# Kernel tuning notes

Measured on AMD Instinct MI355X. Metric: run time of the kernel, lower is better.

Reference implementation:

```python
import jax, jax.numpy as jnp
import numpy as np

TEMPERATURE = 0.5

def setup_inputs() -> dict:
    key = jax.random.key(0)
    k1, k2 = jax.random.split(key)
    N, D = 4096, 128
    emb_i = jax.random.normal(k1, (N, D), dtype=jnp.float32)
    emb_j = jax.random.normal(k2, (N, D), dtype=jnp.float32)
    return {"emb_i": emb_i, "emb_j": emb_j}

def reference(emb_i, emb_j):
    # L2-normalize each embedding (F.normalize, dim=1)
    z_i = emb_i / jnp.linalg.norm(emb_i, axis=1, keepdims=True)
    z_j = emb_j / jnp.linalg.norm(emb_j, axis=1, keepdims=True)
    N = z_j.shape[0]
    reps = jnp.concatenate([z_i, z_j], axis=0)  # [2N, D], unit rows
    # cosine similarity of unit vectors == dot product
    logits = jnp.einsum('id,jd->ij', reps, reps) / TEMPERATURE  # [2N, 2N]
    # denominator excludes only k == i (self), positive pair included
    diag_mask = jnp.eye(2 * N, dtype=bool)
    masked = jnp.where(diag_mask, -jnp.inf, logits)
    lse = jax.nn.logsumexp(masked, axis=1)  # [2N]
    # positive index: i <-> i+N
    pos_idx = jnp.concatenate([jnp.arange(N) + N, jnp.arange(N)])
    pos_logits = jnp.take_along_axis(logits, pos_idx[:, None], axis=1)[:, 0]
    # loss = mean over all 2N anchors of -(log numerator - log denominator)
    loss = jnp.mean(lse - pos_logits)
    return loss
```

## Files before the change

### kernel.cpp

```cpp
#include <hip/hip_runtime.h>
#include <hip/hip_bf16.h>

#define NROW 4096
#define D 128
#define TOT 8192
#define PRESCALE 1.69864407f

typedef __attribute__((ext_vector_type(8))) short bf16x8;
typedef __attribute__((ext_vector_type(4))) float f32x4;

__device__ __forceinline__ float fast_exp2(float x) {
#if __has_builtin(__builtin_amdgcn_exp2f)
  return __builtin_amdgcn_exp2f(x);
#else
  return exp2f(x);
#endif
}
__device__ __forceinline__ float fast_log2(float x) {
#if __has_builtin(__builtin_amdgcn_logf)
  return __builtin_amdgcn_logf(x);
#else
  return log2f(x);
#endif
}

__device__ __forceinline__ unsigned short f2bf(float x) {
  unsigned u = __float_as_uint(x);
  unsigned r = (u + 0x7fffu + ((u >> 16) & 1u)) >> 16;
  return (unsigned short)r;
}

__global__ __launch_bounds__(256) void k_norm(
    const float* __restrict__ ei, const float* __restrict__ ej,
    unsigned short* __restrict__ Zp, float* __restrict__ pos) {
  int wid = threadIdx.x >> 6;
  int lane = threadIdx.x & 63;
  int r = blockIdx.x * 4 + wid;
  const float2 xi = *(const float2*)(ei + (size_t)r * D + lane * 2);
  const float2 xj = *(const float2*)(ej + (size_t)r * D + lane * 2);
  float si = xi.x * xi.x + xi.y * xi.y;
  float sj = xj.x * xj.x + xj.y * xj.y;
  float dd = xi.x * xj.x + xi.y * xj.y;
#pragma unroll
  for (int m = 32; m >= 1; m >>= 1) {
    si += __shfl_xor(si, m, 64);
    sj += __shfl_xor(sj, m, 64);
    dd += __shfl_xor(dd, m, 64);
  }
  float ri = rsqrtf(si); ri = ri * (1.5f - 0.5f * si * ri * ri);
  float rj = rsqrtf(sj); rj = rj * (1.5f - 0.5f * sj * rj * rj);
  unsigned short a0 = f2bf(xi.x * ri * PRESCALE);
  unsigned short a1 = f2bf(xi.y * ri * PRESCALE);
  unsigned short b0 = f2bf(xj.x * rj * PRESCALE);
  unsigned short b1 = f2bf(xj.y * rj * PRESCALE);
  unsigned wa = (unsigned)a0 | ((unsigned)a1 << 16);
  unsigned wb = (unsigned)b0 | ((unsigned)b1 << 16);
  ((unsigned*)(Zp + (size_t)r * D))[lane] = wa;
  ((unsigned*)(Zp + (size_t)(r + NROW) * D))[lane] = wb;
  if (lane == 0) pos[r] = 2.0f * dd * ri * rj;
}

#define RG 32
#define CS 32
#define CPB (TOT / CS)
__global__ __launch_bounds__(256) void k_gemm(
    const unsigned short* __restrict__ Zp, float* __restrict__ rowsum) {
  int wid = threadIdx.x >> 6;
  int lane = threadIdx.x & 63;
  int lo = lane & 15, hi = lane >> 4;
  int rb = blockIdx.x & (RG - 1);
  int cs = blockIdx.x >> 5;
  int rowbase = rb * 256 + wid * 64;

  bf16x8 af[4][4];
#pragma unroll
  for (int g = 0; g < 4; ++g) {
    const unsigned short* za = Zp + (size_t)(rowbase + g * 16 + lo) * D + hi * 8;
#pragma unroll
    for (int kk = 0; kk < 4; ++kk)
      af[g][kk] = *(const bf16x8*)(za + kk * 32);
  }

  float sums[4][4];
#pragma unroll
  for (int g = 0; g < 4; ++g)
#pragma unroll
    for (int r = 0; r < 4; ++r) sums[g][r] = 0.0f;

  bool blkdiag = (cs == rb);
#pragma unroll 4
  for (int t = 0; t < CPB / 16; ++t) {
    int colbase = cs * CPB + t * 16;
    const unsigned short* zb = Zp + (size_t)(colbase + lo) * D + hi * 8;
    bf16x8 bf[4];
#pragma unroll
    for (int kk = 0; kk < 4; ++kk)
      bf[kk] = *(const bf16x8*)(zb + kk * 32);
    int gd = t - wid * 4;
#pragma unroll
    for (int g = 0; g < 4; ++g) {
      f32x4 acc = {0.0f, 0.0f, 0.0f, 0.0f};
#pragma unroll
      for (int kk = 0; kk < 4; ++kk)
        acc = __builtin_amdgcn_mfma_f32_16x16x32_bf16(af[g][kk], bf[kk], acc, 0, 0, 0);
      if (blkdiag && g == gd) {
#pragma unroll
        for (int r = 0; r < 4; ++r) {
          float e = (lo == hi * 4 + r) ? 0.0f : fast_exp2(acc[r]);
          sums[g][r] += e;
        }
      } else {
#pragma unroll
        for (int r = 0; r < 4; ++r) sums[g][r] += fast_exp2(acc[r]);
      }
    }
  }

#pragma unroll
  for (int g = 0; g < 4; ++g)
#pragma unroll
    for (int r = 0; r < 4; ++r) {
      float v = sums[g][r];
      v += __shfl_xor(v, 1, 64);
      v += __shfl_xor(v, 2, 64);
      v += __shfl_xor(v, 4, 64);
      v += __shfl_xor(v, 8, 64);
      if (lo == 0) atomicAdd(&rowsum[rowbase + g * 16 + hi * 4 + r], v);
    }
}

__global__ __launch_bounds__(256) void k_final(
    const float* __restrict__ rowsum, const float* __restrict__ pos,
    float* __restrict__ out) {
  int idx = blockIdx.x * 256 + (int)threadIdx.x;
  float lse = fast_log2(rowsum[idx]) * 0.69314718055994531f;
  float c = lse * (1.0f / (float)TOT);
  if (idx < NROW) c -= pos[idx] * (1.0f / (float)NROW);
#pragma unroll
  for (int m = 32; m >= 1; m >>= 1) c += __shfl_xor(c, m, 64);
  __shared__ float ws[4];
  int wid = threadIdx.x >> 6, lane = threadIdx.x & 63;
  if (lane == 0) ws[wid] = c;
  __syncthreads();
  if (threadIdx.x == 0) atomicAdd(out, ws[0] + ws[1] + ws[2] + ws[3]);
}

extern "C" void kernel_launch(void* const* d_in, const int* in_sizes, int n_in,
                              void* d_out, int out_size, void* d_ws, size_t ws_size,
                              hipStream_t stream) {
  const float* ei = (const float*)d_in[0];
  const float* ej = (const float*)d_in[1];
  float* out = (float*)d_out;
  float* rowsum = (float*)d_ws;
  float* pos = (float*)((char*)d_ws + TOT * 4);
  unsigned short* Zp =
      (unsigned short*)((char*)d_ws + TOT * 4 + NROW * 4);

  hipMemsetAsync(out, 0, sizeof(float), stream);
  hipMemsetAsync(rowsum, 0, TOT * sizeof(float), stream);
  k_norm<<<NROW / 4, 256, 0, stream>>>(ei, ej, Zp, pos);
  k_gemm<<<RG * CS, 256, 0, stream>>>(Zp, rowsum);
  k_final<<<TOT / 256, 256, 0, stream>>>(rowsum, pos, out);
}
```

Before: 108.0 us.

## Stage column tiles via async LDS loads, fuse finalize, drop memsets

```diff
diff --git a/kernel.cpp b/kernel.cpp
--- a/kernel.cpp
+++ b/kernel.cpp
@@ -5,6 +5,9 @@
 #define D 128
 #define TOT 8192
 #define PRESCALE 1.69864407f
+#define GRID_G 1024
+#define CPB 256
+#define NT 16
 
 typedef __attribute__((ext_vector_type(8))) short bf16x8;
 typedef __attribute__((ext_vector_type(4))) float f32x4;
@@ -30,9 +33,20 @@
   return (unsigned short)r;
 }
 
+__device__ __forceinline__ void gload16(const void* g, void* l) {
+  __builtin_amdgcn_global_load_lds(
+      (const __attribute__((address_space(1))) unsigned int*)g,
+      (__attribute__((address_space(3))) unsigned int*)l, 16, 0, 0);
+}
+
 __global__ __launch_bounds__(256) void k_norm(
     const float* __restrict__ ei, const float* __restrict__ ej,
-    unsigned short* __restrict__ Zp, float* __restrict__ pos) {
+    unsigned short* __restrict__ Zp, float* __restrict__ pos,
+    float* __restrict__ rowsum, unsigned* __restrict__ ctr) {
+  int gid = blockIdx.x * 256 + (int)threadIdx.x;
+  if (gid < TOT) rowsum[gid] = 0.0f;
+  if (gid == TOT) *ctr = 0u;
+
   int wid = threadIdx.x >> 6;
   int lane = threadIdx.x & 63;
   int r = blockIdx.x * 4 + wid;
@@ -53,33 +67,42 @@
   unsigned short a1 = f2bf(xi.y * ri * PRESCALE);
   unsigned short b0 = f2bf(xj.x * rj * PRESCALE);
   unsigned short b1 = f2bf(xj.y * rj * PRESCALE);
-  unsigned wa = (unsigned)a0 | ((unsigned)a1 << 16);
-  unsigned wb = (unsigned)b0 | ((unsigned)b1 << 16);
-  ((unsigned*)(Zp + (size_t)r * D))[lane] = wa;
-  ((unsigned*)(Zp + (size_t)(r + NROW) * D))[lane] = wb;
+  ((unsigned*)(Zp + (size_t)r * D))[lane] = (unsigned)a0 | ((unsigned)a1 << 16);
+  ((unsigned*)(Zp + (size_t)(r + NROW) * D))[lane] = (unsigned)b0 | ((unsigned)b1 << 16);
   if (lane == 0) pos[r] = 2.0f * dd * ri * rj;
 }
 
-#define RG 32
-#define CS 32
-#define CPB (TOT / CS)
-__global__ __launch_bounds__(256) void k_gemm(
-    const unsigned short* __restrict__ Zp, float* __restrict__ rowsum) {
-  int wid = threadIdx.x >> 6;
-  int lane = threadIdx.x & 63;
-  int lo = lane & 15, hi = lane >> 4;
-  int rb = blockIdx.x & (RG - 1);
-  int cs = blockIdx.x >> 5;
-  int rowbase = rb * 256 + wid * 64;
+__global__ __launch_bounds__(256, 4) void k_gemm(
+    const unsigned short* __restrict__ Zp, float* __restrict__ rowsum,
+    const float* __restrict__ pos, unsigned* __restrict__ ctr,
+    float* __restrict__ out) {
+  __shared__ __align__(16) char ldsb[8192];
+  const int tid = (int)threadIdx.x;
+  const int wid = tid >> 6, lane = tid & 63;
+  const int lo = lane & 15, hi = lane >> 4;
+  const unsigned b = blockIdx.x;
+  const int cs = (int)((b & 7u) * 4u + ((b >> 3) & 3u));
+  const int rb = (int)(b >> 5);
+  const int rowbase = rb * 256 + wid * 64;
 
   bf16x8 af[4][4];
 #pragma unroll
   for (int g = 0; g < 4; ++g) {
     const unsigned short* za = Zp + (size_t)(rowbase + g * 16 + lo) * D + hi * 8;
 #pragma unroll
-    for (int kk = 0; kk < 4; ++kk)
-      af[g][kk] = *(const bf16x8*)(za + kk * 32);
-  }
+    for (int kk = 0; kk < 4; ++kk) af[g][kk] = *(const bf16x8*)(za + kk * 32);
+  }
+
+  int rdoff[4];
+  const int sw = (lo & 7) << 4;
+#pragma unroll
+  for (int kk = 0; kk < 4; ++kk) rdoff[kk] = lo * 256 + (((kk * 4 + hi) * 16) ^ sw);
+
+  const int Rr = wid * 4 + (lane >> 4);
+  const int B0 = (lane & 15) * 16;
+  const char* gbase = (const char*)Zp + (size_t)cs * CPB * 256 +
+                      (size_t)Rr * 256 + (size_t)(B0 ^ ((Rr & 7) << 4));
+  char* ldsw = ldsb + wid * 1024;
 
   float sums[4][4];
 #pragma unroll
@@ -87,33 +110,43 @@
 #pragma unroll
     for (int r = 0; r < 4; ++r) sums[g][r] = 0.0f;
 
-  bool blkdiag = (cs == rb);
-#pragma unroll 4
-  for (int t = 0; t < CPB / 16; ++t) {
-    int colbase = cs * CPB + t * 16;
-    const unsigned short* zb = Zp + (size_t)(colbase + lo) * D + hi * 8;
-    bf16x8 bf[4];
-#pragma unroll
-    for (int kk = 0; kk < 4; ++kk)
-      bf[kk] = *(const bf16x8*)(zb + kk * 32);
-    int gd = t - wid * 4;
-#pragma unroll
-    for (int g = 0; g < 4; ++g) {
-      f32x4 acc = {0.0f, 0.0f, 0.0f, 0.0f};
-#pragma unroll
-      for (int kk = 0; kk < 4; ++kk)
-        acc = __builtin_amdgcn_mfma_f32_16x16x32_bf16(af[g][kk], bf[kk], acc, 0, 0, 0);
-      if (blkdiag && g == gd) {
-#pragma unroll
-        for (int r = 0; r < 4; ++r) {
-          float e = (lo == hi * 4 + r) ? 0.0f : fast_exp2(acc[r]);
-          sums[g][r] += e;
-        }
-      } else {
-#pragma unroll
-        for (int r = 0; r < 4; ++r) sums[g][r] += fast_exp2(acc[r]);
+  const bool blkdiag = (cs == rb);
+
+  gload16(gbase, ldsw);
+  asm volatile("s_waitcnt vmcnt(0)" ::: "memory");
+
+#pragma unroll 2
+  for (int t = 0; t < NT; ++t) {
+    if (t + 1 < NT) {
+      gload16(gbase + (size_t)(t + 1) * 4096, ldsw + ((t + 1) & 1) * 4096);
+      asm volatile("s_waitcnt vmcnt(1)" ::: "memory");
+    } else {
+      asm volatile("s_waitcnt vmcnt(0)" ::: "memory");
+    }
+    __builtin_amdgcn_s_barrier();
+
+    const char* ldsr = ldsb + (t & 1) * 4096;
+    f32x4 acc[4];
+#pragma unroll
+    for (int g = 0; g < 4; ++g) acc[g] = (f32x4){0.f, 0.f, 0.f, 0.f};
+#pragma unroll
+    for (int kk = 0; kk < 4; ++kk) {
+      bf16x8 bfv = *(const bf16x8*)(ldsr + rdoff[kk]);
+#pragma unroll
+      for (int g = 0; g < 4; ++g)
+        acc[g] = __builtin_amdgcn_mfma_f32_16x16x32_bf16(af[g][kk], bfv, acc[g], 0, 0, 0);
+    }
+    const int gd = blkdiag ? (t - wid * 4) : -1;
+#pragma unroll
+    for (int g = 0; g < 4; ++g)
+#pragma unroll
+      for (int r = 0; r < 4; ++r) {
+        float e = fast_exp2(acc[g][r]);
+        sums[g][r] += (g == gd && lo == hi * 4 + r) ? 0.0f : e;
       }
-    }
+    asm volatile("s_waitcnt lgkmcnt(0)" ::: "memory");
+    __builtin_amdgcn_sched_barrier(0);
+    __builtin_amdgcn_s_barrier();
   }
 
 #pragma unroll
@@ -127,22 +160,29 @@
       v += __shfl_xor(v, 8, 64);
       if (lo == 0) atomicAdd(&rowsum[rowbase + g * 16 + hi * 4 + r], v);
     }
-}
-
-__global__ __launch_bounds__(256) void k_final(
-    const float* __restrict__ rowsum, const float* __restrict__ pos,
-    float* __restrict__ out) {
-  int idx = blockIdx.x * 256 + (int)threadIdx.x;
-  float lse = fast_log2(rowsum[idx]) * 0.69314718055994531f;
-  float c = lse * (1.0f / (float)TOT);
-  if (idx < NROW) c -= pos[idx] * (1.0f / (float)NROW);
-#pragma unroll
-  for (int m = 32; m >= 1; m >>= 1) c += __shfl_xor(c, m, 64);
-  __shared__ float ws[4];
-  int wid = threadIdx.x >> 6, lane = threadIdx.x & 63;
-  if (lane == 0) ws[wid] = c;
+
   __syncthreads();
-  if (threadIdx.x == 0) atomicAdd(out, ws[0] + ws[1] + ws[2] + ws[3]);
+  __shared__ unsigned slast;
+  if (tid == 0) {
+    __threadfence();
+    slast = atomicAdd(ctr, 1u);
+  }
+  __syncthreads();
+  if (slast == GRID_G - 1) {
+    float s1 = 0.0f, s2 = 0.0f;
+    for (int k = tid; k < TOT; k += 256) {
+      float v = __hip_atomic_load(&rowsum[k], __ATOMIC_RELAXED, __HIP_MEMORY_SCOPE_AGENT);
+      s1 += fast_log2(v);
+    }
+    for (int k = tid; k < NROW; k += 256) s2 += pos[k];
+    float c = s1 * (0.69314718055994531f / (float)TOT) - s2 * (1.0f / (float)NROW);
+#pragma unroll
+    for (int m = 32; m >= 1; m >>= 1) c += __shfl_xor(c, m, 64);
+    __shared__ float wsum[4];
+    if (lane == 0) wsum[wid] = c;
+    __syncthreads();
+    if (tid == 0) out[0] = wsum[0] + wsum[1] + wsum[2] + wsum[3];
+  }
 }
 
 extern "C" void kernel_launch(void* const* d_in, const int* in_sizes, int n_in,
@@ -153,12 +193,10 @@
   float* out = (float*)d_out;
   float* rowsum = (float*)d_ws;
   float* pos = (float*)((char*)d_ws + TOT * 4);
+  unsigned* ctr = (unsigned*)((char*)d_ws + TOT * 4 + NROW * 4);
   unsigned short* Zp =
-      (unsigned short*)((char*)d_ws + TOT * 4 + NROW * 4);
-
-  hipMemsetAsync(out, 0, sizeof(float), stream);
-  hipMemsetAsync(rowsum, 0, TOT * sizeof(float), stream);
-  k_norm<<<NROW / 4, 256, 0, stream>>>(ei, ej, Zp, pos);
-  k_gemm<<<RG * CS, 256, 0, stream>>>(Zp, rowsum);
-  k_final<<<TOT / 256, 256, 0, stream>>>(rowsum, pos, out);
-}
+      (unsigned short*)((char*)d_ws + TOT * 4 + NROW * 4 + 256);
+
+  k_norm<<<NROW / 4, 256, 0, stream>>>(ei, ej, Zp, pos, rowsum, ctr);
+  k_gemm<<<GRID_G, 256, 0, stream>>>(Zp, rowsum, pos, ctr, out);
+}
```

Measured after the change: 108.5 us. About the same (+0.5%).
